# Kernel tuning notes

Hardware: AMD Instinct MI355X
Metric: run time of the kernel (lower is better)

## Reference

```python
import math
import jax, jax.numpy as jnp
import numpy as np

B = 64
INPUT_SIZE = 10080
PATCH = 18
S = INPUT_SIZE // PATCH  # 560 patches
E = 96                    # embed_dim
H = 12                    # num_heads
D = 96                    # head_dim == embed_dim (PAT quirk)
F = 256                   # ff_dim
L = 2                     # num_layers
EPS = 1e-5


def _sinusoidal_pe(seq_len, embed_dim):
    pos = jnp.arange(seq_len, dtype=jnp.float32)[:, None]
    div = jnp.exp(jnp.arange(0, embed_dim, 2, dtype=jnp.float32) * (-math.log(10000.0) / embed_dim))
    pe = jnp.zeros((seq_len, embed_dim), dtype=jnp.float32)
    pe = pe.at[:, 0::2].set(jnp.sin(pos * div))
    pe = pe.at[:, 1::2].set(jnp.cos(pos * div))
    return pe


def _layernorm(x, g, b):
    mu = jnp.mean(x, axis=-1, keepdims=True)
    var = jnp.var(x, axis=-1, keepdims=True)
    return (x - mu) * jax.lax.rsqrt(var + EPS) * g + b


def setup_inputs() -> dict:
    key = jax.random.key(0)
    ks = jax.random.split(key, 12)
    sd = 0.02
    inp = {
        "x": jax.random.normal(ks[0], (B, INPUT_SIZE), dtype=jnp.float32),
        "patch_W": jax.random.normal(ks[1], (PATCH, E), dtype=jnp.float32) * sd,
        "patch_b": jnp.zeros((E,), jnp.float32),
        "Wq": jax.random.normal(ks[2], (L, H, E, D), dtype=jnp.float32) * sd,
        "bq": jnp.zeros((L, H, D), jnp.float32),
        "Wk": jax.random.normal(ks[3], (L, H, E, D), dtype=jnp.float32) * sd,
        "bk": jnp.zeros((L, H, D), jnp.float32),
        "Wv": jax.random.normal(ks[4], (L, H, E, D), dtype=jnp.float32) * sd,
        "bv": jnp.zeros((L, H, D), jnp.float32),
        "Wo": jax.random.normal(ks[5], (L, H * D, E), dtype=jnp.float32) * sd,
        "bo": jnp.zeros((L, E), jnp.float32),
        "ff1_W": jax.random.normal(ks[6], (L, E, F), dtype=jnp.float32) * sd,
        "ff1_b": jnp.zeros((L, F), jnp.float32),
        "ff2_W": jax.random.normal(ks[7], (L, F, E), dtype=jnp.float32) * sd,
        "ff2_b": jnp.zeros((L, E), jnp.float32),
        "n1_g": jnp.ones((L, E), jnp.float32),
        "n1_b": jnp.zeros((L, E), jnp.float32),
        "n2_g": jnp.ones((L, E), jnp.float32),
        "n2_b": jnp.zeros((L, E), jnp.float32),
    }
    return inp


def reference(x, patch_W, patch_b, Wq, bq, Wk, bk, Wv, bv, Wo, bo,
              ff1_W, ff1_b, ff2_W, ff2_b, n1_g, n1_b, n2_g, n2_b):
    scale = 1.0 / math.sqrt(D)
    # patch embedding: [B, S, PATCH] -> [B, S, E]
    h = x.reshape(B, S, PATCH) @ patch_W + patch_b
    h = h + _sinusoidal_pe(S, E)[None]
    for l in range(L):
        # all heads at once (original loops over heads; same math)
        q = jnp.einsum('bse,hed->bhsd', h, Wq[l]) + bq[l][None, :, None, :]
        k = jnp.einsum('bse,hed->bhsd', h, Wk[l]) + bk[l][None, :, None, :]
        v = jnp.einsum('bse,hed->bhsd', h, Wv[l]) + bv[l][None, :, None, :]
        scores = jnp.einsum('bhsd,bhtd->bhst', q, k) * scale
        attn = jax.nn.softmax(scores, axis=-1)
        heads = jnp.einsum('bhst,bhtd->bhsd', attn, v)
        concat = heads.transpose(0, 2, 1, 3).reshape(B, S, H * D)
        attn_out = concat @ Wo[l] + bo[l]
        h = _layernorm(h + attn_out, n1_g[l], n1_b[l])
        ff = jax.nn.relu(h @ ff1_W[l] + ff1_b[l]) @ ff2_W[l] + ff2_b[l]
        h = _layernorm(h + ff, n2_g[l], n2_b[l])
    return h
```

## Files before the change

kernel.cpp:

```cpp
#include <hip/hip_runtime.h>
#include <hip/hip_bf16.h>
#include <math.h>

#define BATCH 64
#define CHUNK 32
#define INPUT_SIZE 10080
#define PATCH 18
#define SEQ 560
#define EMB 96
#define NHEAD 12
#define HDIM 96
#define FFDIM 256
#define NLAYER 2
#define TOK (BATCH * SEQ)
#define EPSV 1e-5f
#define SCALE 0.10206207261596577f

typedef __attribute__((ext_vector_type(8))) short bf16x8;
typedef __attribute__((ext_vector_type(4))) short bf16x4;
typedef __attribute__((ext_vector_type(4))) float f32x4;

static __device__ __forceinline__ short f2bf(float x) {
  union { __hip_bfloat16 b; short s; } u;
  u.b = __float2bfloat16(x);
  return u.s;
}

__global__ __launch_bounds__(256) void wprep_kernel(
    const float* __restrict__ Wq, const float* __restrict__ Wk,
    const float* __restrict__ Wv, __hip_bfloat16* __restrict__ wqT,
    __hip_bfloat16* __restrict__ wkvT) {
  int hh = blockIdx.x, mat = blockIdx.y, l = blockIdx.z;
  const float* src =
      (mat == 0 ? Wq : (mat == 1 ? Wk : Wv)) + ((size_t)l * NHEAD + hh) * EMB * HDIM;
  __shared__ float t[HDIM * 97];
  for (int i = threadIdx.x; i < EMB * HDIM; i += 256) {
    int e = i / HDIM, d = i % HDIM;
    t[d * 97 + e] = src[i];
  }
  __syncthreads();
  __hip_bfloat16* dst;
  if (mat == 0)
    dst = wqT + ((size_t)l * NHEAD + hh) * HDIM * EMB;
  else
    dst = wkvT + ((size_t)l * 2 * NHEAD * HDIM + (mat - 1) * NHEAD * HDIM +
                  hh * HDIM) * EMB;
  for (int j = threadIdx.x; j < HDIM * EMB; j += 256) {
    int d = j / EMB, e = j % EMB;
    dst[j] = __float2bfloat16(t[d * 97 + e]);
  }
}

__global__ __launch_bounds__(256) void woprep_kernel(
    const float* __restrict__ Wo, __hip_bfloat16* __restrict__ woT) {
  int l = blockIdx.x;
  const float* src = Wo + (size_t)l * NHEAD * HDIM * EMB;
  __hip_bfloat16* dst = woT + (size_t)l * EMB * NHEAD * HDIM;
  for (int i = threadIdx.x; i < EMB * NHEAD * HDIM; i += 256) {
    int e = i / (NHEAD * HDIM), j = i % (NHEAD * HDIM);
    dst[i] = __float2bfloat16(src[(size_t)j * EMB + e]);
  }
}

__global__ __launch_bounds__(256) void ffprep_kernel(
    const float* __restrict__ ff1_W, const float* __restrict__ ff2_W,
    __hip_bfloat16* __restrict__ ff1WT, __hip_bfloat16* __restrict__ ff2WT) {
  int mat = blockIdx.x, l = blockIdx.y;
  if (mat == 0) {
    const float* src = ff1_W + (size_t)l * EMB * FFDIM;
    __hip_bfloat16* dst = ff1WT + (size_t)l * FFDIM * EMB;
    for (int i = threadIdx.x; i < FFDIM * EMB; i += 256) {
      int f = i / EMB, e = i % EMB;
      dst[i] = __float2bfloat16(src[(size_t)e * FFDIM + f]);
    }
  } else {
    const float* src = ff2_W + (size_t)l * FFDIM * EMB;
    __hip_bfloat16* dst = ff2WT + (size_t)l * EMB * FFDIM;
    for (int i = threadIdx.x; i < EMB * FFDIM; i += 256) {
      int e = i / FFDIM, f = i % FFDIM;
      dst[i] = __float2bfloat16(src[(size_t)f * EMB + e]);
    }
  }
}

__global__ void patch_pe_kernel(const float* __restrict__ x,
                                const float* __restrict__ W,
                                const float* __restrict__ bias,
                                float* __restrict__ h,
                                __hip_bfloat16* __restrict__ hbf) {
  int gid = blockIdx.x * blockDim.x + threadIdx.x;
  if (gid >= TOK * EMB) return;
  int tok = gid / EMB;
  int e = gid % EMB;
  int b = tok / SEQ;
  int s = tok % SEQ;
  const float* xp = x + b * INPUT_SIZE + s * PATCH;
  float acc = bias[e];
#pragma unroll
  for (int p = 0; p < PATCH; p++) acc += xp[p] * W[p * EMB + e];
  int i = e >> 1;
  float freq = __expf(-(float)(2 * i) * (9.210340371976184f / 96.0f));
  float ang = (float)s * freq;
  acc += (e & 1) ? cosf(ang) : sinf(ang);
  h[gid] = acc;
  hbf[gid] = __float2bfloat16(acc);
}

__global__ __launch_bounds__(256) void kv_mfma_kernel(
    const __hip_bfloat16* __restrict__ hbf,
    const __hip_bfloat16* __restrict__ wkvT, const float* __restrict__ bk,
    const float* __restrict__ bv, __hip_bfloat16* __restrict__ kbuf,
    __hip_bfloat16* __restrict__ vbufT, int b0) {
  const int wave = threadIdx.x >> 6;
  const int lane = threadIdx.x & 63;
  const int tq = lane & 15;
  const int quad = lane >> 4;
  const int m0 = blockIdx.x * 64 + wave * 16;
  const int n0 = blockIdx.y * 64;

  const short* ap =
      (const short*)hbf + ((size_t)b0 * SEQ + m0 + tq) * EMB + quad * 8;
  bf16x8 a0 = *(const bf16x8*)(ap);
  bf16x8 a1 = *(const bf16x8*)(ap + 32);
  bf16x8 a2 = *(const bf16x8*)(ap + 64);

  f32x4 acc[4];
  const f32x4 zero4 = {0.f, 0.f, 0.f, 0.f};
#pragma unroll
  for (int nt = 0; nt < 4; nt++) acc[nt] = zero4;
#pragma unroll
  for (int nt = 0; nt < 4; nt++) {
    const short* bp =
        (const short*)wkvT + (size_t)(n0 + nt * 16 + tq) * EMB + quad * 8;
    bf16x8 b0f = *(const bf16x8*)(bp);
    bf16x8 b1f = *(const bf16x8*)(bp + 32);
    bf16x8 b2f = *(const bf16x8*)(bp + 64);
    acc[nt] = __builtin_amdgcn_mfma_f32_16x16x32_bf16(a0, b0f, acc[nt], 0, 0, 0);
    acc[nt] = __builtin_amdgcn_mfma_f32_16x16x32_bf16(a1, b1f, acc[nt], 0, 0, 0);
    acc[nt] = __builtin_amdgcn_mfma_f32_16x16x32_bf16(a2, b2f, acc[nt], 0, 0, 0);
  }

  const int tl0 = m0 + quad * 4;
  const int blb = tl0 / SEQ;
  const int ss0 = tl0 - blb * SEQ;
#pragma unroll
  for (int nt = 0; nt < 4; nt++) {
    int n = n0 + nt * 16 + tq;
    int kv = n / (NHEAD * HDIM);
    int r = n - kv * (NHEAD * HDIM);
    int hh = r / HDIM;
    int d = r - hh * HDIM;
    if (kv) {
      float bias = bv[r];
      bf16x4 pack;
#pragma unroll
      for (int j = 0; j < 4; j++) pack[j] = f2bf(acc[nt][j] + bias);
      *(bf16x4*)((short*)vbufT +
                 ((size_t)(blb * NHEAD + hh) * HDIM + d) * SEQ + ss0) = pack;
    } else {
      float bias = bk[r];
#pragma unroll
      for (int j = 0; j < 4; j++) {
        kbuf[((size_t)(blb * NHEAD + hh) * SEQ + ss0 + j) * HDIM + d] =
            __float2bfloat16(acc[nt][j] + bias);
      }
    }
  }
}

#define PSTRIDE 584
#define KSTR 104
__global__ __launch_bounds__(256, 2) void attn_mfma_kernel(
    const __hip_bfloat16* __restrict__ hbf,
    const __hip_bfloat16* __restrict__ wqT, const float* __restrict__ bq,
    const __hip_bfloat16* __restrict__ kbuf,
    const __hip_bfloat16* __restrict__ vbufT,
    __hip_bfloat16* __restrict__ heads, int b0) {
  const int flat = blockIdx.x;
  const int xcd = flat & 7;
  const int slot = flat >> 3;
  const int g = (slot / 9) * 8 + xcd;
  const int qt = slot % 9;
  const int hh = g % NHEAD;
  const int bl = g / NHEAD;
  const int wave = threadIdx.x >> 6;
  const int lane = threadIdx.x & 63;
  const int tq = lane & 15;
  const int quad = lane >> 4;

  __shared__ __align__(16) short sbuf[4 * 16 * PSTRIDE];
  short* pw = sbuf + wave * 16 * PSTRIDE;

  const size_t bh = (size_t)(bl * NHEAD + hh);
  const short* kb = (const short*)kbuf + bh * SEQ * HDIM;
  const short* vb = (const short*)vbufT + bh * HDIM * SEQ;

  const int q0 = qt * 64 + wave * 16;
  int qrow = q0 + tq;
  if (qrow > SEQ - 1) qrow = SEQ - 1;
  const short* hp =
      (const short*)hbf + ((size_t)(b0 + bl) * SEQ + qrow) * EMB + quad * 8;
  bf16x8 ha0 = *(const bf16x8*)(hp);
  bf16x8 ha1 = *(const bf16x8*)(hp + 32);
  bf16x8 ha2 = *(const bf16x8*)(hp + 64);
  const f32x4 zero4 = {0.f, 0.f, 0.f, 0.f};
  f32x4 qacc[6];
#pragma unroll
  for (int dt = 0; dt < 6; dt++) qacc[dt] = zero4;
#pragma unroll
  for (int dt = 0; dt < 6; dt++) {
    const short* wp = (const short*)wqT +
                      ((size_t)hh * HDIM + dt * 16 + tq) * EMB + quad * 8;
    bf16x8 w0 = *(const bf16x8*)(wp);
    bf16x8 w1 = *(const bf16x8*)(wp + 32);
    bf16x8 w2 = *(const bf16x8*)(wp + 64);
    qacc[dt] = __builtin_amdgcn_mfma_f32_16x16x32_bf16(ha0, w0, qacc[dt], 0, 0, 0);
    qacc[dt] = __builtin_amdgcn_mfma_f32_16x16x32_bf16(ha1, w1, qacc[dt], 0, 0, 0);
    qacc[dt] = __builtin_amdgcn_mfma_f32_16x16x32_bf16(ha2, w2, qacc[dt], 0, 0, 0);
  }
#pragma unroll
  for (int dt = 0; dt < 6; dt++) {
    int d = dt * 16 + tq;
    float bias = bq[hh * HDIM + d];
#pragma unroll
    for (int r = 0; r < 4; r++)
      pw[(quad * 4 + r) * PSTRIDE + d] = f2bf((qacc[dt][r] + bias) * SCALE);
  }
  bf16x8 aq0 = *(const bf16x8*)&pw[tq * PSTRIDE + quad * 8];
  bf16x8 aq1 = *(const bf16x8*)&pw[tq * PSTRIDE + quad * 8 + 32];
  bf16x8 aq2 = *(const bf16x8*)&pw[tq * PSTRIDE + quad * 8 + 64];
  __syncthreads();

  f32x4 acc[35];
#pragma unroll
  for (int tt = 0; tt < 35; tt++) acc[tt] = zero4;

  for (int i = threadIdx.x; i < 288 * 12; i += 256) {
    int row = i / 12, gg = i - row * 12;
    *(bf16x8*)&sbuf[row * KSTR + gg * 8] =
        *(const bf16x8*)(kb + (size_t)row * HDIM + gg * 8);
  }
  __syncthreads();
#pragma unroll
  for (int tt = 0; tt < 18; tt++) {
    const short* kp = &sbuf[(tt * 16 + tq) * KSTR + quad * 8];
    bf16x8 kb0 = *(const bf16x8*)(kp);
    bf16x8 kb1 = *(const bf16x8*)(kp + 32);
    bf16x8 kb2 = *(const bf16x8*)(kp + 64);
    acc[tt] = __builtin_amdgcn_mfma_f32_16x16x32_bf16(aq0, kb0, acc[tt], 0, 0, 0);
    acc[tt] = __builtin_amdgcn_mfma_f32_16x16x32_bf16(aq1, kb1, acc[tt], 0, 0, 0);
    acc[tt] = __builtin_amdgcn_mfma_f32_16x16x32_bf16(aq2, kb2, acc[tt], 0, 0, 0);
  }
  __syncthreads();

  for (int i = threadIdx.x; i < 272 * 12; i += 256) {
    int row = i / 12, gg = i - row * 12;
    *(bf16x8*)&sbuf[row * KSTR + gg * 8] =
        *(const bf16x8*)(kb + (size_t)(288 + row) * HDIM + gg * 8);
  }
  __syncthreads();
#pragma unroll
  for (int tt = 18; tt < 35; tt++) {
    const short* kp = &sbuf[(tt * 16 + tq - 288) * KSTR + quad * 8];
    bf16x8 kb0 = *(const bf16x8*)(kp);
    bf16x8 kb1 = *(const bf16x8*)(kp + 32);
    bf16x8 kb2 = *(const bf16x8*)(kp + 64);
    acc[tt] = __builtin_amdgcn_mfma_f32_16x16x32_bf16(aq0, kb0, acc[tt], 0, 0, 0);
    acc[tt] = __builtin_amdgcn_mfma_f32_16x16x32_bf16(aq1, kb1, acc[tt], 0, 0, 0);
    acc[tt] = __builtin_amdgcn_mfma_f32_16x16x32_bf16(aq2, kb2, acc[tt], 0, 0, 0);
  }

  float m0 = -1e30f, m1 = -1e30f, m2 = -1e30f, m3 = -1e30f;
#pragma unroll
  for (int tt = 0; tt < 35; tt++) {
    m0 = fmaxf(m0, acc[tt][0]);
    m1 = fmaxf(m1, acc[tt][1]);
    m2 = fmaxf(m2, acc[tt][2]);
    m3 = fmaxf(m3, acc[tt][3]);
  }
#pragma unroll
  for (int mask = 1; mask < 16; mask <<= 1) {
    m0 = fmaxf(m0, __shfl_xor(m0, mask, 64));
    m1 = fmaxf(m1, __shfl_xor(m1, mask, 64));
    m2 = fmaxf(m2, __shfl_xor(m2, mask, 64));
    m3 = fmaxf(m3, __shfl_xor(m3, mask, 64));
  }
  float l0 = 0.f, l1 = 0.f, l2 = 0.f, l3 = 0.f;
#pragma unroll
  for (int tt = 0; tt < 35; tt++) {
    float p0 = __expf(acc[tt][0] - m0); acc[tt][0] = p0; l0 += p0;
    float p1 = __expf(acc[tt][1] - m1); acc[tt][1] = p1; l1 += p1;
    float p2 = __expf(acc[tt][2] - m2); acc[tt][2] = p2; l2 += p2;
    float p3 = __expf(acc[tt][3] - m3); acc[tt][3] = p3; l3 += p3;
  }
#pragma unroll
  for (int mask = 1; mask < 16; mask <<= 1) {
    l0 += __shfl_xor(l0, mask, 64);
    l1 += __shfl_xor(l1, mask, 64);
    l2 += __shfl_xor(l2, mask, 64);
    l3 += __shfl_xor(l3, mask, 64);
  }
  __syncthreads();

  for (int i = lane; i < 256; i += 64)
    pw[(i >> 4) * PSTRIDE + 560 + (i & 15)] = 0;
#pragma unroll
  for (int tt = 0; tt < 35; tt++) {
    int col = tt * 16 + tq;
    pw[(quad * 4 + 0) * PSTRIDE + col] = f2bf(acc[tt][0]);
    pw[(quad * 4 + 1) * PSTRIDE + col] = f2bf(acc[tt][1]);
    pw[(quad * 4 + 2) * PSTRIDE + col] = f2bf(acc[tt][2]);
    pw[(quad * 4 + 3) * PSTRIDE + col] = f2bf(acc[tt][3]);
  }

  f32x4 oacc[6];
#pragma unroll
  for (int dt = 0; dt < 6; dt++) oacc[dt] = zero4;
#pragma unroll
  for (int kt = 0; kt < 18; kt++) {
    bf16x8 pa = *(const bf16x8*)&pw[tq * PSTRIDE + kt * 32 + quad * 8];
#pragma unroll
    for (int dt = 0; dt < 6; dt++) {
      const short* vp = vb + (size_t)(dt * 16 + tq) * SEQ + kt * 32 + quad * 8;
      bf16x8 vf = *(const bf16x8*)vp;
      oacc[dt] = __builtin_amdgcn_mfma_f32_16x16x32_bf16(pa, vf, oacc[dt], 0, 0, 0);
    }
  }

  float r0 = 1.f / l0, r1 = 1.f / l1, r2 = 1.f / l2, r3 = 1.f / l3;
  int qg = q0 + quad * 4;
  __hip_bfloat16* hpout =
      heads + ((size_t)(b0 + bl) * SEQ) * (NHEAD * HDIM) + (size_t)hh * HDIM;
#pragma unroll
  for (int dt = 0; dt < 6; dt++) {
    int d = dt * 16 + tq;
    if (qg + 0 < SEQ) hpout[(size_t)(qg + 0) * (NHEAD * HDIM) + d] = __float2bfloat16(oacc[dt][0] * r0);
    if (qg + 1 < SEQ) hpout[(size_t)(qg + 1) * (NHEAD * HDIM) + d] = __float2bfloat16(oacc[dt][1] * r1);
    if (qg + 2 < SEQ) hpout[(size_t)(qg + 2) * (NHEAD * HDIM) + d] = __float2bfloat16(oacc[dt][2] * r2);
    if (qg + 3 < SEQ) hpout[(size_t)(qg + 3) * (NHEAD * HDIM) + d] = __float2bfloat16(oacc[dt][3] * r3);
  }
}

__global__ __launch_bounds__(256) void wo_ln_mfma_kernel(
    const __hip_bfloat16* __restrict__ heads,
    const __hip_bfloat16* __restrict__ woT, const float* __restrict__ bo,
    const float* __restrict__ gamma, const float* __restrict__ beta,
    const float* __restrict__ hres, float* __restrict__ hA,
    __hip_bfloat16* __restrict__ hbf) {
  const int wave = threadIdx.x >> 6;
  const int lane = threadIdx.x & 63;
  const int tq = lane & 15;
  const int quad = lane >> 4;
  const int m0 = blockIdx.x * 64 + wave * 16;

  const short* ap = (const short*)heads + (size_t)(m0 + tq) * (NHEAD * HDIM);
  const short* bp = (const short*)woT;

  f32x4 acc[6];
  const f32x4 zero4 = {0.f, 0.f, 0.f, 0.f};
#pragma unroll
  for (int dt = 0; dt < 6; dt++) acc[dt] = zero4;

  for (int kt = 0; kt < 36; kt++) {
    bf16x8 af = *(const bf16x8*)(ap + kt * 32 + quad * 8);
#pragma unroll
    for (int dt = 0; dt < 6; dt++) {
      bf16x8 bfr = *(const bf16x8*)(bp + (size_t)(dt * 16 + tq) * (NHEAD * HDIM) +
                                    kt * 32 + quad * 8);
      acc[dt] = __builtin_amdgcn_mfma_f32_16x16x32_bf16(af, bfr, acc[dt], 0, 0, 0);
    }
  }

  const int tok0 = m0 + quad * 4;
  float s1[4] = {0.f, 0.f, 0.f, 0.f};
  float s2[4] = {0.f, 0.f, 0.f, 0.f};
#pragma unroll
  for (int dt = 0; dt < 6; dt++) {
    int n = dt * 16 + tq;
    float bias = bo[n];
#pragma unroll
    for (int r = 0; r < 4; r++) {
      float val = acc[dt][r] + bias + hres[(size_t)(tok0 + r) * EMB + n];
      acc[dt][r] = val;
      s1[r] += val;
      s2[r] += val * val;
    }
  }
#pragma unroll
  for (int mask = 1; mask < 16; mask <<= 1) {
#pragma unroll
    for (int r = 0; r < 4; r++) {
      s1[r] += __shfl_xor(s1[r], mask, 64);
      s2[r] += __shfl_xor(s2[r], mask, 64);
    }
  }
  float mean[4], rstd[4];
#pragma unroll
  for (int r = 0; r < 4; r++) {
    mean[r] = s1[r] * (1.0f / EMB);
    float var = s2[r] * (1.0f / EMB) - mean[r] * mean[r];
    rstd[r] = rsqrtf(var + EPSV);
  }
#pragma unroll
  for (int dt = 0; dt < 6; dt++) {
    int n = dt * 16 + tq;
    float g = gamma[n], bt = beta[n];
#pragma unroll
    for (int r = 0; r < 4; r++) {
      float o = (acc[dt][r] - mean[r]) * rstd[r] * g + bt;
      hA[(size_t)(tok0 + r) * EMB + n] = o;
      hbf[(size_t)(tok0 + r) * EMB + n] = __float2bfloat16(o);
    }
  }
}

__global__ __launch_bounds__(256) void ff1_mfma_kernel(
    const __hip_bfloat16* __restrict__ hbf,
    const __hip_bfloat16* __restrict__ ff1WT, const float* __restrict__ b1,
    __hip_bfloat16* __restrict__ ffbf) {
  const int wave = threadIdx.x >> 6;
  const int lane = threadIdx.x & 63;
  const int tq = lane & 15;
  const int quad = lane >> 4;
  const int m0 = blockIdx.x * 64 + wave * 16;

  const short* ap = (const short*)hbf + (size_t)(m0 + tq) * EMB + quad * 8;
  bf16x8 a0 = *(const bf16x8*)(ap);
  bf16x8 a1 = *(const bf16x8*)(ap + 32);
  bf16x8 a2 = *(const bf16x8*)(ap + 64);

  f32x4 acc[16];
  const f32x4 zero4 = {0.f, 0.f, 0.f, 0.f};
#pragma unroll
  for (int nt = 0; nt < 16; nt++) acc[nt] = zero4;
#pragma unroll
  for (int nt = 0; nt < 16; nt++) {
    const short* bp =
        (const short*)ff1WT + (size_t)(nt * 16 + tq) * EMB + quad * 8;
    bf16x8 b0f = *(const bf16x8*)(bp);
    bf16x8 b1f = *(const bf16x8*)(bp + 32);
    bf16x8 b2f = *(const bf16x8*)(bp + 64);
    acc[nt] = __builtin_amdgcn_mfma_f32_16x16x32_bf16(a0, b0f, acc[nt], 0, 0, 0);
    acc[nt] = __builtin_amdgcn_mfma_f32_16x16x32_bf16(a1, b1f, acc[nt], 0, 0, 0);
    acc[nt] = __builtin_amdgcn_mfma_f32_16x16x32_bf16(a2, b2f, acc[nt], 0, 0, 0);
  }

  const int tok0 = m0 + quad * 4;
#pragma unroll
  for (int nt = 0; nt < 16; nt++) {
    int n = nt * 16 + tq;
    float bias = b1[n];
#pragma unroll
    for (int r = 0; r < 4; r++) {
      ffbf[(size_t)(tok0 + r) * FFDIM + n] =
          __float2bfloat16(fmaxf(acc[nt][r] + bias, 0.f));
    }
  }
}

__global__ __launch_bounds__(256) void ff2_ln_mfma_kernel(
    const __hip_bfloat16* __restrict__ ffbf,
    const __hip_bfloat16* __restrict__ ff2WT, const float* __restrict__ b2,
    const float* __restrict__ gamma, const float* __restrict__ beta,
    const float* __restrict__ hres, float* __restrict__ hout,
    __hip_bfloat16* __restrict__ hbf_out) {
  const int wave = threadIdx.x >> 6;
  const int lane = threadIdx.x & 63;
  const int tq = lane & 15;
  const int quad = lane >> 4;
  const int m0 = blockIdx.x * 64 + wave * 16;

  const short* ap = (const short*)ffbf + (size_t)(m0 + tq) * FFDIM;
  const short* bp = (const short*)ff2WT;

  f32x4 acc[6];
  const f32x4 zero4 = {0.f, 0.f, 0.f, 0.f};
#pragma unroll
  for (int dt = 0; dt < 6; dt++) acc[dt] = zero4;

#pragma unroll
  for (int kt = 0; kt < 8; kt++) {
    bf16x8 af = *(const bf16x8*)(ap + kt * 32 + quad * 8);
#pragma unroll
    for (int dt = 0; dt < 6; dt++) {
      bf16x8 bfr = *(const bf16x8*)(bp + (size_t)(dt * 16 + tq) * FFDIM +
                                    kt * 32 + quad * 8);
      acc[dt] = __builtin_amdgcn_mfma_f32_16x16x32_bf16(af, bfr, acc[dt], 0, 0, 0);
    }
  }

  const int tok0 = m0 + quad * 4;
  float s1[4] = {0.f, 0.f, 0.f, 0.f};
  float s2[4] = {0.f, 0.f, 0.f, 0.f};
#pragma unroll
  for (int dt = 0; dt < 6; dt++) {
    int n = dt * 16 + tq;
    float bias = b2[n];
#pragma unroll
    for (int r = 0; r < 4; r++) {
      float val = acc[dt][r] + bias + hres[(size_t)(tok0 + r) * EMB + n];
      acc[dt][r] = val;
      s1[r] += val;
      s2[r] += val * val;
    }
  }
#pragma unroll
  for (int mask = 1; mask < 16; mask <<= 1) {
#pragma unroll
    for (int r = 0; r < 4; r++) {
      s1[r] += __shfl_xor(s1[r], mask, 64);
      s2[r] += __shfl_xor(s2[r], mask, 64);
    }
  }
  float mean[4], rstd[4];
#pragma unroll
  for (int r = 0; r < 4; r++) {
    mean[r] = s1[r] * (1.0f / EMB);
    float var = s2[r] * (1.0f / EMB) - mean[r] * mean[r];
    rstd[r] = rsqrtf(var + EPSV);
  }
#pragma unroll
  for (int dt = 0; dt < 6; dt++) {
    int n = dt * 16 + tq;
    float g = gamma[n], bt = beta[n];
#pragma unroll
    for (int r = 0; r < 4; r++) {
      float o = (acc[dt][r] - mean[r]) * rstd[r] * g + bt;
      hout[(size_t)(tok0 + r) * EMB + n] = o;
      hbf_out[(size_t)(tok0 + r) * EMB + n] = __float2bfloat16(o);
    }
  }
}

extern "C" void kernel_launch(void* const* d_in, const int* in_sizes, int n_in,
                              void* d_out, int out_size, void* d_ws,
                              size_t ws_size, hipStream_t stream) {
  const float* x = (const float*)d_in[0];
  const float* patch_W = (const float*)d_in[1];
  const float* patch_b = (const float*)d_in[2];
  const float* Wq = (const float*)d_in[3];
  const float* bq = (const float*)d_in[4];
  const float* Wk = (const float*)d_in[5];
  const float* bk = (const float*)d_in[6];
  const float* Wv = (const float*)d_in[7];
  const float* bv = (const float*)d_in[8];
  const float* Wo = (const float*)d_in[9];
  const float* bo = (const float*)d_in[10];
  const float* ff1_W = (const float*)d_in[11];
  const float* ff1_b = (const float*)d_in[12];
  const float* ff2_W = (const float*)d_in[13];
  const float* ff2_b = (const float*)d_in[14];
  const float* n1_g = (const float*)d_in[15];
  const float* n1_b = (const float*)d_in[16];
  const float* n2_g = (const float*)d_in[17];
  const float* n2_b = (const float*)d_in[18];

  const size_t h_bytes = (size_t)TOK * EMB * sizeof(float);
  const size_t hbf_bytes = (size_t)TOK * EMB * 2;
  const size_t kv_bytes = (size_t)CHUNK * NHEAD * SEQ * HDIM * 2;
  const size_t heads_bytes = (size_t)TOK * NHEAD * HDIM * 2;
  const size_t wqT_bytes = (size_t)NLAYER * NHEAD * HDIM * EMB * 2;
  const size_t wkvT_bytes = 2 * wqT_bytes;
  const size_t woT_bytes = (size_t)NLAYER * EMB * NHEAD * HDIM * 2;
  const size_t ffw_bytes = (size_t)NLAYER * FFDIM * EMB * 2;
  char* ws = (char*)d_ws;
  size_t off = 0;
  float* h = (float*)(ws + off); off += h_bytes;
  float* hA = (float*)(ws + off); off += h_bytes;
  __hip_bfloat16* hbf = (__hip_bfloat16*)(ws + off); off += hbf_bytes;
  __hip_bfloat16* kbuf = (__hip_bfloat16*)(ws + off); off += kv_bytes;
  __hip_bfloat16* vbufT = (__hip_bfloat16*)(ws + off); off += kv_bytes;
  __hip_bfloat16* heads = (__hip_bfloat16*)(ws + off); off += heads_bytes;
  __hip_bfloat16* wqT = (__hip_bfloat16*)(ws + off); off += wqT_bytes;
  __hip_bfloat16* wkvT = (__hip_bfloat16*)(ws + off); off += wkvT_bytes;
  __hip_bfloat16* woT = (__hip_bfloat16*)(ws + off); off += woT_bytes;
  __hip_bfloat16* ff1WT = (__hip_bfloat16*)(ws + off); off += ffw_bytes;
  __hip_bfloat16* ff2WT = (__hip_bfloat16*)(ws + off); off += ffw_bytes;
  __hip_bfloat16* ffbf = (__hip_bfloat16*)kbuf;

  wprep_kernel<<<dim3(NHEAD, 3, NLAYER), 256, 0, stream>>>(Wq, Wk, Wv, wqT, wkvT);
  woprep_kernel<<<NLAYER, 256, 0, stream>>>(Wo, woT);
  ffprep_kernel<<<dim3(2, NLAYER), 256, 0, stream>>>(ff1_W, ff2_W, ff1WT, ff2WT);
  patch_pe_kernel<<<(TOK * EMB + 255) / 256, 256, 0, stream>>>(x, patch_W,
                                                               patch_b, h, hbf);

  for (int l = 0; l < NLAYER; l++) {
    const __hip_bfloat16* wqT_l = wqT + (size_t)l * NHEAD * HDIM * EMB;
    const __hip_bfloat16* wkvT_l = wkvT + (size_t)l * 2 * NHEAD * HDIM * EMB;
    const __hip_bfloat16* woT_l = woT + (size_t)l * EMB * NHEAD * HDIM;
    const __hip_bfloat16* ff1WT_l = ff1WT + (size_t)l * FFDIM * EMB;
    const __hip_bfloat16* ff2WT_l = ff2WT + (size_t)l * EMB * FFDIM;
    const float* bq_l = bq + (size_t)l * NHEAD * HDIM;
    const float* bk_l = bk + (size_t)l * NHEAD * HDIM;
    const float* bv_l = bv + (size_t)l * NHEAD * HDIM;
    const float* bo_l = bo + (size_t)l * EMB;

    for (int c = 0; c < BATCH / CHUNK; c++) {
      int b0 = c * CHUNK;
      kv_mfma_kernel<<<dim3(CHUNK * SEQ / 64, 2 * NHEAD * HDIM / 64), 256, 0,
                       stream>>>(hbf, wkvT_l, bk_l, bv_l, kbuf, vbufT, b0);
      attn_mfma_kernel<<<9 * NHEAD * CHUNK, 256, 0, stream>>>(
          hbf, wqT_l, bq_l, kbuf, vbufT, heads, b0);
    }
    wo_ln_mfma_kernel<<<TOK / 64, 256, 0, stream>>>(
        heads, woT_l, bo_l, n1_g + l * EMB, n1_b + l * EMB, h, hA, hbf);
    ff1_mfma_kernel<<<TOK / 64, 256, 0, stream>>>(hbf, ff1WT_l,
                                                  ff1_b + l * FFDIM, ffbf);
    float* dst = (l == NLAYER - 1) ? (float*)d_out : h;
    ff2_ln_mfma_kernel<<<TOK / 64, 256, 0, stream>>>(
        ffbf, ff2WT_l, ff2_b + l * EMB, n2_g + l * EMB, n2_b + l * EMB, hA,
        dst, hbf);
  }
}
```

Measured before the change: 1.415 ms.

## Split PV matmul across waves by K range and reduce partials through LDS

The P·V product in the attention kernel is restructured so that each wave computes all four 16-row query tiles over its own slice of the key dimension, rather than each wave handling its own 16 rows over the full key range. Each V fragment loaded from global memory is therefore reused across four MFMAs, cutting redundant V loads per block by about four times. Partial outputs are exchanged through shared memory and summed per wave. This adds extra barriers and LDS traffic and raises register pressure with 24 accumulators, which may reduce occupancy.

```diff
diff --git a/kernel.cpp b/kernel.cpp
--- a/kernel.cpp
+++ b/kernel.cpp
@@ -312,21 +312,59 @@
     pw[(quad * 4 + 2) * PSTRIDE + col] = f2bf(acc[tt][2]);
     pw[(quad * 4 + 3) * PSTRIDE + col] = f2bf(acc[tt][3]);
   }
-
-  f32x4 oacc[6];
-#pragma unroll
-  for (int dt = 0; dt < 6; dt++) oacc[dt] = zero4;
-#pragma unroll
-  for (int kt = 0; kt < 18; kt++) {
-    bf16x8 pa = *(const bf16x8*)&pw[tq * PSTRIDE + kt * 32 + quad * 8];
+  __syncthreads();
+
+  const int kts[4] = {0, 5, 10, 14};
+  const int kte[4] = {5, 10, 14, 18};
+  f32x4 oacc[4][6];
+#pragma unroll
+  for (int mt = 0; mt < 4; mt++)
+#pragma unroll
+    for (int dt = 0; dt < 6; dt++) oacc[mt][dt] = zero4;
+  for (int kt = kts[wave]; kt < kte[wave]; kt++) {
+    bf16x8 pa[4];
+#pragma unroll
+    for (int mt = 0; mt < 4; mt++)
+      pa[mt] = *(const bf16x8*)&sbuf[(mt * 16 + tq) * PSTRIDE + kt * 32 + quad * 8];
 #pragma unroll
     for (int dt = 0; dt < 6; dt++) {
       const short* vp = vb + (size_t)(dt * 16 + tq) * SEQ + kt * 32 + quad * 8;
       bf16x8 vf = *(const bf16x8*)vp;
-      oacc[dt] = __builtin_amdgcn_mfma_f32_16x16x32_bf16(pa, vf, oacc[dt], 0, 0, 0);
-    }
-  }
-
+#pragma unroll
+      for (int mt = 0; mt < 4; mt++)
+        oacc[mt][dt] =
+            __builtin_amdgcn_mfma_f32_16x16x32_bf16(pa[mt], vf, oacc[mt][dt], 0, 0, 0);
+    }
+  }
+  __syncthreads();
+
+  float* redf = (float*)sbuf;
+#pragma unroll
+  for (int mt = 0; mt < 4; mt++) {
+    if (mt == wave) continue;
+    int sr = (wave < mt) ? wave : wave - 1;
+#pragma unroll
+    for (int dt = 0; dt < 6; dt++) {
+#pragma unroll
+      for (int r = 0; r < 4; r++)
+        redf[((mt * 3 + sr) * 16 + quad * 4 + r) * 97 + dt * 16 + tq] =
+            oacc[mt][dt][r];
+    }
+  }
+  __syncthreads();
+
+  f32x4 fin[6];
+#pragma unroll
+  for (int dt = 0; dt < 6; dt++) {
+    fin[dt] = oacc[wave][dt];
+#pragma unroll
+    for (int sr = 0; sr < 3; sr++) {
+#pragma unroll
+      for (int r = 0; r < 4; r++)
+        fin[dt][r] +=
+            redf[((wave * 3 + sr) * 16 + quad * 4 + r) * 97 + dt * 16 + tq];
+    }
+  }
   float r0 = 1.f / l0, r1 = 1.f / l1, r2 = 1.f / l2, r3 = 1.f / l3;
   int qg = q0 + quad * 4;
   __hip_bfloat16* hpout =
@@ -334,10 +372,10 @@
 #pragma unroll
   for (int dt = 0; dt < 6; dt++) {
     int d = dt * 16 + tq;
-    if (qg + 0 < SEQ) hpout[(size_t)(qg + 0) * (NHEAD * HDIM) + d] = __float2bfloat16(oacc[dt][0] * r0);
-    if (qg + 1 < SEQ) hpout[(size_t)(qg + 1) * (NHEAD * HDIM) + d] = __float2bfloat16(oacc[dt][1] * r1);
-    if (qg + 2 < SEQ) hpout[(size_t)(qg + 2) * (NHEAD * HDIM) + d] = __float2bfloat16(oacc[dt][2] * r2);
-    if (qg + 3 < SEQ) hpout[(size_t)(qg + 3) * (NHEAD * HDIM) + d] = __float2bfloat16(oacc[dt][3] * r3);
+    if (qg + 0 < SEQ) hpout[(size_t)(qg + 0) * (NHEAD * HDIM) + d] = __float2bfloat16(fin[dt][0] * r0);
+    if (qg + 1 < SEQ) hpout[(size_t)(qg + 1) * (NHEAD * HDIM) + d] = __float2bfloat16(fin[dt][1] * r1);
+    if (qg + 2 < SEQ) hpout[(size_t)(qg + 2) * (NHEAD * HDIM) + d] = __float2bfloat16(fin[dt][2] * r2);
+    if (qg + 3 < SEQ) hpout[(size_t)(qg + 3) * (NHEAD * HDIM) + d] = __float2bfloat16(fin[dt][3] * r3);
   }
 }
 
```

Result: slower. 1.615 ms (+14.1%).
